# Performance work log

Hardware: AMD Instinct MI355X
Metric: run time of the kernel (lower is better)

## Reference

```python
import jax, jax.numpy as jnp
import numpy as np

NUM_HEADS = 16

def setup_inputs() -> dict:
    key = jax.random.key(0)
    k1, k2, k3 = jax.random.split(key, 3)
    D = 1024
    return {
        "hidden_states": jax.random.normal(k1, (2, 2048, D), dtype=jnp.float32),
        "c_attn_w": jax.random.normal(k2, (D, 3 * D), dtype=jnp.float32) * 0.02,
        "c_attn_b": jnp.zeros((3 * D,), dtype=jnp.float32),
        "c_proj_w": jax.random.normal(k3, (D, D), dtype=jnp.float32) * 0.02,
        "c_proj_b": jnp.zeros((D,), dtype=jnp.float32),
    }

def reference(hidden_states, c_attn_w, c_attn_b, c_proj_w, c_proj_b):
    B, S, D = hidden_states.shape
    H = NUM_HEADS
    hd = D // H
    # Conv1D: x @ W + b, then split into q, k, v
    qkv = hidden_states @ c_attn_w + c_attn_b  # [B, S, 3D]
    q, k, v = jnp.split(qkv, 3, axis=-1)
    q = q.reshape(B, S, H, hd).transpose(0, 2, 1, 3)  # [B, H, S, hd]
    k = k.reshape(B, S, H, hd).transpose(0, 2, 1, 3)
    v = v.reshape(B, S, H, hd).transpose(0, 2, 1, 3)
    # scaled QK^T
    scores = jnp.einsum("bhqd,bhkd->bhqk", q, k) / jnp.asarray(hd ** 0.5, q.dtype)
    # causal mask (tril), masked positions set to dtype min per original code
    causal = jnp.tril(jnp.ones((S, S), dtype=bool))
    mask_value = jnp.finfo(scores.dtype).min
    scores = jnp.where(causal[None, None], scores, mask_value)
    attn = jax.nn.softmax(scores, axis=-1)
    out = jnp.einsum("bhqk,bhkd->bhqd", attn, v)  # [B, H, S, hd]
    out = out.transpose(0, 2, 1, 3).reshape(B, S, D)
    out = out @ c_proj_w + c_proj_b
    return out
```

## Files before the change

### kernel.cpp

```cpp
#include <hip/hip_runtime.h>
#include <hip/hip_bf16.h>
#include <math.h>

#define B_ 2
#define S_ 2048
#define D_ 1024
#define H_ 16
#define HD 64
#define M_ (B_ * S_)
#define N_QKV (3 * D_)

typedef short short8 __attribute__((ext_vector_type(8)));
typedef float floatx4 __attribute__((ext_vector_type(4)));

static __device__ __forceinline__ unsigned short f2bf(float x) {
    __hip_bfloat16 h = __float2bfloat16(x);
    unsigned short u;
    __builtin_memcpy(&u, &h, sizeof(u));
    return u;
}
static __device__ __forceinline__ float bf2f(unsigned short b) {
    union { unsigned u; float f; } v; v.u = ((unsigned)b) << 16;
    return v.f;
}
static __device__ __forceinline__ void split2(float x, unsigned short& h, unsigned short& l) {
    h = f2bf(x);
    l = f2bf(x - bf2f(h));
}

static __device__ __forceinline__ void dma16(const void* g, void* l) {
    __builtin_amdgcn_global_load_lds(
        (const __attribute__((address_space(1))) unsigned int*)g,
        (__attribute__((address_space(3))) unsigned int*)l,
        16, 0, 0);
}

__global__ __launch_bounds__(256) void prep_A(
    const float* __restrict__ X,
    unsigned short* __restrict__ Ahi, unsigned short* __restrict__ Alo)
{
    const size_t i = ((size_t)blockIdx.x * 256 + threadIdx.x) * 8;
    float4 a = *(const float4*)(X + i);
    float4 b = *(const float4*)(X + i + 4);
    float xs[8] = {a.x, a.y, a.z, a.w, b.x, b.y, b.z, b.w};
    short8 h, l;
#pragma unroll
    for (int e = 0; e < 8; e++) {
        unsigned short hh, ll;
        split2(xs[e], hh, ll);
        h[e] = (short)hh; l[e] = (short)ll;
    }
    *(short8*)&Ahi[i] = h;
    *(short8*)&Alo[i] = l;
}

__global__ __launch_bounds__(256) void prep_wT(
    const float* __restrict__ W, int N,
    unsigned short* __restrict__ Thi, unsigned short* __restrict__ Tlo)
{
    __shared__ float Ws[64][68];
    const int t  = threadIdx.x;
    const int n0 = blockIdx.x * 64, k0 = blockIdx.y * 64;
    {
        const int kl = t >> 4, nl = (t & 15) * 4;
        const float* src = W + (size_t)(k0 + kl) * N + n0 + nl;
#pragma unroll
        for (int g = 0; g < 4; g++)
            *(float4*)&Ws[kl + g * 16][nl] = *(const float4*)(src + (size_t)g * 16 * N);
    }
    __syncthreads();
    {
        const int nl = t >> 2, ks = (t & 3) * 16;
        short8 h0, h1, l0, l1;
#pragma unroll
        for (int j = 0; j < 8; j++) {
            unsigned short hh, ll;
            split2(Ws[ks + j][nl], hh, ll);
            h0[j] = (short)hh; l0[j] = (short)ll;
        }
#pragma unroll
        for (int j = 0; j < 8; j++) {
            unsigned short hh, ll;
            split2(Ws[ks + 8 + j][nl], hh, ll);
            h1[j] = (short)hh; l1[j] = (short)ll;
        }
        unsigned short* dh = Thi + (size_t)(n0 + nl) * D_ + k0 + ks;
        unsigned short* dl = Tlo + (size_t)(n0 + nl) * D_ + k0 + ks;
        *(short8*)dh = h0; *(short8*)(dh + 8) = h1;
        *(short8*)dl = l0; *(short8*)(dl + 8) = l1;
    }
}

__global__ __launch_bounds__(256) void gemm_qkv(
    const unsigned short* __restrict__ Ahi, const unsigned short* __restrict__ Alo,
    const unsigned short* __restrict__ BThi, const unsigned short* __restrict__ BTlo,
    const float* __restrict__ bias,
    unsigned short* __restrict__ Qhi, unsigned short* __restrict__ Qlo,
    unsigned short* __restrict__ Khi, unsigned short* __restrict__ Klo,
    unsigned short* __restrict__ vThi, unsigned short* __restrict__ vTlo)
{
    __shared__ unsigned short sAh[128 * 32], sAl[128 * 32];
    __shared__ unsigned short sBh[128 * 32], sBl[128 * 32];

    const int t    = threadIdx.x;
    const int m0   = blockIdx.y * 128, n0 = blockIdx.x * 128;
    const int lane = t & 63, wave = t >> 6;
    const int lm   = lane & 15, quad = lane >> 4;
    const int wm   = (wave >> 1) * 64, wn = (wave & 1) * 64;

    const int lrow = lane >> 2, lcol = (lane & 3) * 8;
    const unsigned short* gAh = Ahi + (size_t)(m0 + wave * 32 + lrow) * D_ + lcol;
    const unsigned short* gAl = Alo + (size_t)(m0 + wave * 32 + lrow) * D_ + lcol;
    const unsigned short* gBh = BThi + (size_t)(n0 + wave * 32 + lrow) * D_ + lcol;
    const unsigned short* gBl = BTlo + (size_t)(n0 + wave * 32 + lrow) * D_ + lcol;
    const int ldst = wave * 1024 + lane * 8;

    floatx4 acc[4][4];
#pragma unroll
    for (int i = 0; i < 4; i++)
#pragma unroll
        for (int j = 0; j < 4; j++)
#pragma unroll
            for (int r = 0; r < 4; r++) acc[i][j][r] = 0.f;

    for (int k0 = 0; k0 < D_; k0 += 32) {
        __syncthreads();
        dma16(gAh + k0, &sAh[ldst]);
        dma16(gAh + (size_t)16 * D_ + k0, &sAh[ldst + 512]);
        dma16(gAl + k0, &sAl[ldst]);
        dma16(gAl + (size_t)16 * D_ + k0, &sAl[ldst + 512]);
        dma16(gBh + k0, &sBh[ldst]);
        dma16(gBh + (size_t)16 * D_ + k0, &sBh[ldst + 512]);
        dma16(gBl + k0, &sBl[ldst]);
        dma16(gBl + (size_t)16 * D_ + k0, &sBl[ldst + 512]);
        __syncthreads();

        short8 bhf[4], blf[4];
#pragma unroll
        for (int nb = 0; nb < 4; nb++) {
            const int r = wn + nb * 16 + lm;
            bhf[nb] = *(const short8*)&sBh[r * 32 + quad * 8];
            blf[nb] = *(const short8*)&sBl[r * 32 + quad * 8];
        }
#pragma unroll
        for (int mb = 0; mb < 4; mb++) {
            const int r = wm + mb * 16 + lm;
            short8 ah = *(const short8*)&sAh[r * 32 + quad * 8];
            short8 al = *(const short8*)&sAl[r * 32 + quad * 8];
#pragma unroll
            for (int nb = 0; nb < 4; nb++) {
                acc[mb][nb] = __builtin_amdgcn_mfma_f32_16x16x32_bf16(ah, bhf[nb], acc[mb][nb], 0, 0, 0);
                acc[mb][nb] = __builtin_amdgcn_mfma_f32_16x16x32_bf16(al, bhf[nb], acc[mb][nb], 0, 0, 0);
                acc[mb][nb] = __builtin_amdgcn_mfma_f32_16x16x32_bf16(ah, blf[nb], acc[mb][nb], 0, 0, 0);
            }
        }
    }

    const int nmode = n0 >> 10;
    if (nmode == 0) {
#pragma unroll
        for (int nb = 0; nb < 4; nb++) {
            const int c = n0 + wn + nb * 16 + lm;
            const float bv = bias[c];
#pragma unroll
            for (int mb = 0; mb < 4; mb++) {
                const int rowb = m0 + wm + mb * 16 + quad * 4;
#pragma unroll
                for (int r = 0; r < 4; r++) {
                    unsigned short hh, ll;
                    split2((acc[mb][nb][r] + bv) * 0.125f, hh, ll);
                    Qhi[(size_t)(rowb + r) * D_ + c] = hh;
                    Qlo[(size_t)(rowb + r) * D_ + c] = ll;
                }
            }
        }
    } else if (nmode == 1) {
#pragma unroll
        for (int nb = 0; nb < 4; nb++) {
            const int c = n0 + wn + nb * 16 + lm;
            const float bv = bias[c];
            const int cq = c - 1024;
#pragma unroll
            for (int mb = 0; mb < 4; mb++) {
                const int rowb = m0 + wm + mb * 16 + quad * 4;
#pragma unroll
                for (int r = 0; r < 4; r++) {
                    unsigned short hh, ll;
                    split2(acc[mb][nb][r] + bv, hh, ll);
                    Khi[(size_t)(rowb + r) * D_ + cq] = hh;
                    Klo[(size_t)(rowb + r) * D_ + cq] = ll;
                }
            }
        }
    } else {
#pragma unroll
        for (int nb = 0; nb < 4; nb++) {
            const int c = n0 + wn + nb * 16 + lm;
            const float bv = bias[c];
            const int cq = c - 2048;
            const int hh_ = cq >> 6, dd = cq & 63;
#pragma unroll
            for (int mb = 0; mb < 4; mb++) {
                const int rowb = m0 + wm + mb * 16 + quad * 4;
                const int bb = rowb >> 11, ss = rowb & 2047;
                unsigned short hv[4], lv[4];
#pragma unroll
                for (int r = 0; r < 4; r++)
                    split2(acc[mb][nb][r] + bv, hv[r], lv[r]);
                const size_t idx = ((size_t)((bb * 16 + hh_) * 64 + dd)) * S_ + ss;
                *(uint2*)&vThi[idx] = make_uint2((unsigned)hv[0] | ((unsigned)hv[1] << 16),
                                                 (unsigned)hv[2] | ((unsigned)hv[3] << 16));
                *(uint2*)&vTlo[idx] = make_uint2((unsigned)lv[0] | ((unsigned)lv[1] << 16),
                                                 (unsigned)lv[2] | ((unsigned)lv[3] << 16));
            }
        }
    }
}

__global__ __launch_bounds__(256) void gemm_out(
    const unsigned short* __restrict__ Ahi, const unsigned short* __restrict__ Alo,
    const unsigned short* __restrict__ BThi, const unsigned short* __restrict__ BTlo,
    const float* __restrict__ bias, float* __restrict__ C)
{
    __shared__ unsigned short sAh[64 * 32], sAl[64 * 32];
    __shared__ unsigned short sBh[64 * 32], sBl[64 * 32];

    const int t   = threadIdx.x;
    const int lid = blockIdx.x;
    const int swz = (lid & 7) * 128 + (lid >> 3);
    const int bx  = swz & 15, by = swz >> 4;
    const int m0  = by * 64, n0 = bx * 64;
    const int lane = t & 63, wave = t >> 6;
    const int lm   = lane & 15, quad = lane >> 4;

    const int lrow = lane >> 2, lcol = (lane & 3) * 8;
    const unsigned short* gAh = Ahi + (size_t)(m0 + wave * 16 + lrow) * D_ + lcol;
    const unsigned short* gAl = Alo + (size_t)(m0 + wave * 16 + lrow) * D_ + lcol;
    const unsigned short* gBh = BThi + (size_t)(n0 + wave * 16 + lrow) * D_ + lcol;
    const unsigned short* gBl = BTlo + (size_t)(n0 + wave * 16 + lrow) * D_ + lcol;
    unsigned short* lAh = sAh + wave * 512 + lane * 8;
    unsigned short* lAl = sAl + wave * 512 + lane * 8;
    unsigned short* lBh = sBh + wave * 512 + lane * 8;
    unsigned short* lBl = sBl + wave * 512 + lane * 8;

    floatx4 acc[4];
#pragma unroll
    for (int j = 0; j < 4; j++)
#pragma unroll
        for (int r = 0; r < 4; r++) acc[j][r] = 0.f;

    for (int k0 = 0; k0 < D_; k0 += 32) {
        __syncthreads();
        dma16(gAh + k0, lAh);
        dma16(gAl + k0, lAl);
        dma16(gBh + k0, lBh);
        dma16(gBl + k0, lBl);
        __syncthreads();

        short8 ah = *(const short8*)&sAh[(wave * 16 + lm) * 32 + quad * 8];
        short8 al = *(const short8*)&sAl[(wave * 16 + lm) * 32 + quad * 8];
#pragma unroll
        for (int nb = 0; nb < 4; nb++) {
            short8 bh = *(const short8*)&sBh[(nb * 16 + lm) * 32 + quad * 8];
            short8 bl = *(const short8*)&sBl[(nb * 16 + lm) * 32 + quad * 8];
            acc[nb] = __builtin_amdgcn_mfma_f32_16x16x32_bf16(ah, bh, acc[nb], 0, 0, 0);
            acc[nb] = __builtin_amdgcn_mfma_f32_16x16x32_bf16(al, bh, acc[nb], 0, 0, 0);
            acc[nb] = __builtin_amdgcn_mfma_f32_16x16x32_bf16(ah, bl, acc[nb], 0, 0, 0);
        }
    }

#pragma unroll
    for (int nb = 0; nb < 4; nb++) {
        const int col = n0 + nb * 16 + lm;
        const float bv = bias[col];
#pragma unroll
        for (int r = 0; r < 4; r++) {
            const int row = m0 + wave * 16 + quad * 4 + r;
            C[(size_t)row * D_ + col] = acc[nb][r] + bv;
        }
    }
}

#define PST 72

__global__ __launch_bounds__(256, 2) void flash_attn_mfma(
    unsigned short* QAhi, unsigned short* QAlo,
    const unsigned short* __restrict__ Khi, const unsigned short* __restrict__ Klo,
    const unsigned short* __restrict__ vThi, const unsigned short* __restrict__ vTlo)
{
    __shared__ unsigned short KhS[64 * PST], KlS[64 * PST];
    __shared__ unsigned short VhS[64 * PST], VlS[64 * PST];
    __shared__ unsigned short PhS[64 * PST], PlS[64 * PST];

    const int t    = threadIdx.x;
    const int pj   = blockIdx.x;
    const int bh   = blockIdx.y;
    const int b    = bh >> 4, h = bh & 15;
    const int lane = t & 63, w = t >> 6;
    const int lm   = lane & 15, quad = lane >> 4;

    const int srow = t >> 2;
    const int sseg = (t & 3) * 16;

    const unsigned short* Kh_b = Khi + (size_t)(b * S_) * D_ + h * HD + sseg;
    const unsigned short* Kl_b = Klo + (size_t)(b * S_) * D_ + h * HD + sseg;
    const unsigned short* Vh_b = vThi + ((size_t)((b * 16 + h) * 64 + srow)) * S_ + sseg;
    const unsigned short* Vl_b = vTlo + ((size_t)((b * 16 + h) * 64 + srow)) * S_ + sseg;

    const int sdst = srow * PST + sseg;

    for (int phse = 0; phse < 2; phse++) {
        const int qt = phse ? (31 - pj) : pj;
        const int q0 = qt * 64;
        const int ntiles = qt + 1;

        short8 qh[2], ql[2];
        {
            const size_t qoff = (size_t)(b * S_ + q0 + 16 * w + lm) * D_ + h * HD + quad * 8;
            qh[0] = *(const short8*)&QAhi[qoff];
            qh[1] = *(const short8*)&QAhi[qoff + 32];
            ql[0] = *(const short8*)&QAlo[qoff];
            ql[1] = *(const short8*)&QAlo[qoff + 32];
        }

        float lsum[4] = {0.f, 0.f, 0.f, 0.f};
        floatx4 o[4];
#pragma unroll
        for (int nb = 0; nb < 4; nb++)
#pragma unroll
            for (int r = 0; r < 4; r++) o[nb][r] = 0.f;

        uint4 pkh0, pkh1, pkl0, pkl1, pvh0, pvh1, pvl0, pvl1;
        pkh0 = *(const uint4*)(Kh_b + (size_t)srow * D_);
        pkh1 = *(const uint4*)(Kh_b + (size_t)srow * D_ + 8);
        pkl0 = *(const uint4*)(Kl_b + (size_t)srow * D_);
        pkl1 = *(const uint4*)(Kl_b + (size_t)srow * D_ + 8);
        pvh0 = *(const uint4*)(Vh_b);
        pvh1 = *(const uint4*)(Vh_b + 8);
        pvl0 = *(const uint4*)(Vl_b);
        pvl1 = *(const uint4*)(Vl_b + 8);

        for (int kt = 0; kt < ntiles; kt++) {
            __syncthreads();
            *(uint4*)&KhS[sdst] = pkh0; *(uint4*)&KhS[sdst + 8] = pkh1;
            *(uint4*)&KlS[sdst] = pkl0; *(uint4*)&KlS[sdst + 8] = pkl1;
            *(uint4*)&VhS[sdst] = pvh0; *(uint4*)&VhS[sdst + 8] = pvh1;
            *(uint4*)&VlS[sdst] = pvl0; *(uint4*)&VlS[sdst + 8] = pvl1;
            __syncthreads();

            if (kt + 1 < ntiles) {
                const int k1 = (kt + 1) * 64;
                pkh0 = *(const uint4*)(Kh_b + (size_t)(k1 + srow) * D_);
                pkh1 = *(const uint4*)(Kh_b + (size_t)(k1 + srow) * D_ + 8);
                pkl0 = *(const uint4*)(Kl_b + (size_t)(k1 + srow) * D_);
                pkl1 = *(const uint4*)(Kl_b + (size_t)(k1 + srow) * D_ + 8);
                pvh0 = *(const uint4*)(Vh_b + k1);
                pvh1 = *(const uint4*)(Vh_b + k1 + 8);
                pvl0 = *(const uint4*)(Vl_b + k1);
                pvl1 = *(const uint4*)(Vl_b + k1 + 8);
            }

            floatx4 sa[4];
#pragma unroll
            for (int nb = 0; nb < 4; nb++)
#pragma unroll
                for (int r = 0; r < 4; r++) sa[nb][r] = 0.f;
            __builtin_amdgcn_s_setprio(1);
#pragma unroll
            for (int s = 0; s < 2; s++) {
#pragma unroll
                for (int nb = 0; nb < 4; nb++) {
                    short8 kh = *(const short8*)&KhS[(nb * 16 + lm) * PST + s * 32 + quad * 8];
                    short8 kl = *(const short8*)&KlS[(nb * 16 + lm) * PST + s * 32 + quad * 8];
                    sa[nb] = __builtin_amdgcn_mfma_f32_16x16x32_bf16(qh[s], kh, sa[nb], 0, 0, 0);
                    sa[nb] = __builtin_amdgcn_mfma_f32_16x16x32_bf16(ql[s], kh, sa[nb], 0, 0, 0);
                    sa[nb] = __builtin_amdgcn_mfma_f32_16x16x32_bf16(qh[s], kl, sa[nb], 0, 0, 0);
                }
            }
            __builtin_amdgcn_s_setprio(0);

            const bool diag = (kt == qt);
            const int kbase = kt * 64;
#pragma unroll
            for (int r = 0; r < 4; r++) {
                const int qabs = q0 + 16 * w + 4 * quad + r;
                const int rloc = 16 * w + 4 * quad + r;
#pragma unroll
                for (int nb = 0; nb < 4; nb++) {
                    float p = __expf(sa[nb][r]);
                    if (diag && (kbase + 16 * nb + lm > qabs)) p = 0.f;
                    lsum[r] += p;
                    unsigned short hh, ll;
                    split2(p, hh, ll);
                    PhS[rloc * PST + 16 * nb + lm] = hh;
                    PlS[rloc * PST + 16 * nb + lm] = ll;
                }
            }

            __builtin_amdgcn_s_setprio(1);
#pragma unroll
            for (int ks = 0; ks < 2; ks++) {
                short8 pf = *(const short8*)&PhS[(16 * w + lm) * PST + ks * 32 + quad * 8];
                short8 pg = *(const short8*)&PlS[(16 * w + lm) * PST + ks * 32 + quad * 8];
#pragma unroll
                for (int nb = 0; nb < 4; nb++) {
                    short8 vhf = *(const short8*)&VhS[(16 * nb + lm) * PST + ks * 32 + quad * 8];
                    short8 vlf = *(const short8*)&VlS[(16 * nb + lm) * PST + ks * 32 + quad * 8];
                    o[nb] = __builtin_amdgcn_mfma_f32_16x16x32_bf16(pf, vhf, o[nb], 0, 0, 0);
                    o[nb] = __builtin_amdgcn_mfma_f32_16x16x32_bf16(pg, vhf, o[nb], 0, 0, 0);
                    o[nb] = __builtin_amdgcn_mfma_f32_16x16x32_bf16(pf, vlf, o[nb], 0, 0, 0);
                }
            }
            __builtin_amdgcn_s_setprio(0);
        }

#pragma unroll
        for (int r = 0; r < 4; r++) {
            float l = lsum[r];
            l += __shfl_xor(l, 1);
            l += __shfl_xor(l, 2);
            l += __shfl_xor(l, 4);
            l += __shfl_xor(l, 8);
            const float inv = 1.f / l;
            const size_t rowoff =
                (size_t)(b * S_ + q0 + 16 * w + 4 * quad + r) * D_ + h * HD + lm;
#pragma unroll
            for (int nb = 0; nb < 4; nb++) {
                unsigned short hh, ll;
                split2(o[nb][r] * inv, hh, ll);
                QAhi[rowoff + 16 * nb] = hh;
                QAlo[rowoff + 16 * nb] = ll;
            }
        }
    }
}

extern "C" void kernel_launch(void* const* d_in, const int* in_sizes, int n_in,
                              void* d_out, int out_size, void* d_ws, size_t ws_size,
                              hipStream_t stream)
{
    const float* hs     = (const float*)d_in[0];
    const float* attn_w = (const float*)d_in[1];
    const float* attn_b = (const float*)d_in[2];
    const float* proj_w = (const float*)d_in[3];
    const float* proj_b = (const float*)d_in[4];
    float* outp = (float*)d_out;

    const size_t QE = (size_t)M_ * D_;
    const size_t WQ = (size_t)D_ * N_QKV;
    unsigned short* Qhi   = (unsigned short*)d_ws;
    unsigned short* Qlo   = Qhi + QE;
    unsigned short* Khi   = Qlo + QE;
    unsigned short* Klo   = Khi + QE;
    unsigned short* vThi  = Klo + QE;
    unsigned short* vTlo  = vThi + QE;
    unsigned short* WqThi = vTlo + QE;
    unsigned short* WqTlo = WqThi + WQ;
    unsigned short* WpThi = WqTlo + WQ;
    unsigned short* WpTlo = WpThi + (size_t)D_ * D_;
    unsigned short* Ahi   = WpTlo + (size_t)D_ * D_;
    unsigned short* Alo   = Ahi + QE;

    dim3 blk(256);
    prep_A<<<dim3(M_ * D_ / 2048), blk, 0, stream>>>(hs, Ahi, Alo);
    prep_wT<<<dim3(N_QKV / 64, D_ / 64), blk, 0, stream>>>(attn_w, N_QKV, WqThi, WqTlo);
    prep_wT<<<dim3(D_ / 64, D_ / 64), blk, 0, stream>>>(proj_w, D_, WpThi, WpTlo);
    gemm_qkv<<<dim3(N_QKV / 128, M_ / 128), blk, 0, stream>>>(
        Ahi, Alo, WqThi, WqTlo, attn_b, Qhi, Qlo, Khi, Klo, vThi, vTlo);
    flash_attn_mfma<<<dim3(16, B_ * H_), dim3(256), 0, stream>>>(
        Qhi, Qlo, Khi, Klo, vThi, vTlo);
    gemm_out<<<dim3(1024), blk, 0, stream>>>(
        Qhi, Qlo, WpThi, WpTlo, proj_b, outp);
}
```

Before: 316.3 us.

## Use 128x128 tiles with split-K atomics in output projection GEMM

The output projection GEMM now uses 128x128 block tiles, with each wave computing a 64x64 sub-tile, and splits K into four 256-wide chunks across grid z. Partial sums are combined with float atomicAdd into an output that a new kernel zeroes first, and the bias is added only by the first split. Larger tiles increase register and LDS reuse per MFMA, and split-K keeps the grid at 1024 blocks despite the larger tiles. The cost is an extra zeroing pass, a 4x atomic read-modify-write traffic on the output, and nondeterministic summation order.

```diff
diff --git a/kernel.cpp b/kernel.cpp
--- a/kernel.cpp
+++ b/kernel.cpp
@@ -33,6 +33,12 @@
         (const __attribute__((address_space(1))) unsigned int*)g,
         (__attribute__((address_space(3))) unsigned int*)l,
         16, 0, 0);
+}
+
+__global__ __launch_bounds__(256) void zero_out(float* __restrict__ C)
+{
+    const size_t i = ((size_t)blockIdx.x * 256 + threadIdx.x) * 4;
+    *(float4*)(C + i) = make_float4(0.f, 0.f, 0.f, 0.f);
 }
 
 __global__ __launch_bounds__(256) void prep_A(
@@ -222,61 +228,75 @@
     const unsigned short* __restrict__ BThi, const unsigned short* __restrict__ BTlo,
     const float* __restrict__ bias, float* __restrict__ C)
 {
-    __shared__ unsigned short sAh[64 * 32], sAl[64 * 32];
-    __shared__ unsigned short sBh[64 * 32], sBl[64 * 32];
-
-    const int t   = threadIdx.x;
-    const int lid = blockIdx.x;
-    const int swz = (lid & 7) * 128 + (lid >> 3);
-    const int bx  = swz & 15, by = swz >> 4;
-    const int m0  = by * 64, n0 = bx * 64;
+    __shared__ unsigned short sAh[128 * 32], sAl[128 * 32];
+    __shared__ unsigned short sBh[128 * 32], sBl[128 * 32];
+
+    const int t     = threadIdx.x;
+    const int m0    = blockIdx.y * 128, n0 = blockIdx.x * 128;
+    const int kbase = blockIdx.z * 256;
     const int lane = t & 63, wave = t >> 6;
     const int lm   = lane & 15, quad = lane >> 4;
+    const int wm   = (wave >> 1) * 64, wn = (wave & 1) * 64;
 
     const int lrow = lane >> 2, lcol = (lane & 3) * 8;
-    const unsigned short* gAh = Ahi + (size_t)(m0 + wave * 16 + lrow) * D_ + lcol;
-    const unsigned short* gAl = Alo + (size_t)(m0 + wave * 16 + lrow) * D_ + lcol;
-    const unsigned short* gBh = BThi + (size_t)(n0 + wave * 16 + lrow) * D_ + lcol;
-    const unsigned short* gBl = BTlo + (size_t)(n0 + wave * 16 + lrow) * D_ + lcol;
-    unsigned short* lAh = sAh + wave * 512 + lane * 8;
-    unsigned short* lAl = sAl + wave * 512 + lane * 8;
-    unsigned short* lBh = sBh + wave * 512 + lane * 8;
-    unsigned short* lBl = sBl + wave * 512 + lane * 8;
-
-    floatx4 acc[4];
-#pragma unroll
-    for (int j = 0; j < 4; j++)
-#pragma unroll
-        for (int r = 0; r < 4; r++) acc[j][r] = 0.f;
-
-    for (int k0 = 0; k0 < D_; k0 += 32) {
+    const unsigned short* gAh = Ahi + (size_t)(m0 + wave * 32 + lrow) * D_ + lcol + kbase;
+    const unsigned short* gAl = Alo + (size_t)(m0 + wave * 32 + lrow) * D_ + lcol + kbase;
+    const unsigned short* gBh = BThi + (size_t)(n0 + wave * 32 + lrow) * D_ + lcol + kbase;
+    const unsigned short* gBl = BTlo + (size_t)(n0 + wave * 32 + lrow) * D_ + lcol + kbase;
+    const int ldst = wave * 1024 + lane * 8;
+
+    floatx4 acc[4][4];
+#pragma unroll
+    for (int i = 0; i < 4; i++)
+#pragma unroll
+        for (int j = 0; j < 4; j++)
+#pragma unroll
+            for (int r = 0; r < 4; r++) acc[i][j][r] = 0.f;
+
+    for (int k0 = 0; k0 < 256; k0 += 32) {
         __syncthreads();
-        dma16(gAh + k0, lAh);
-        dma16(gAl + k0, lAl);
-        dma16(gBh + k0, lBh);
-        dma16(gBl + k0, lBl);
+        dma16(gAh + k0, &sAh[ldst]);
+        dma16(gAh + (size_t)16 * D_ + k0, &sAh[ldst + 512]);
+        dma16(gAl + k0, &sAl[ldst]);
+        dma16(gAl + (size_t)16 * D_ + k0, &sAl[ldst + 512]);
+        dma16(gBh + k0, &sBh[ldst]);
+        dma16(gBh + (size_t)16 * D_ + k0, &sBh[ldst + 512]);
+        dma16(gBl + k0, &sBl[ldst]);
+        dma16(gBl + (size_t)16 * D_ + k0, &sBl[ldst + 512]);
         __syncthreads();
 
-        short8 ah = *(const short8*)&sAh[(wave * 16 + lm) * 32 + quad * 8];
-        short8 al = *(const short8*)&sAl[(wave * 16 + lm) * 32 + quad * 8];
+        short8 bhf[4], blf[4];
 #pragma unroll
         for (int nb = 0; nb < 4; nb++) {
-            short8 bh = *(const short8*)&sBh[(nb * 16 + lm) * 32 + quad * 8];
-            short8 bl = *(const short8*)&sBl[(nb * 16 + lm) * 32 + quad * 8];
-            acc[nb] = __builtin_amdgcn_mfma_f32_16x16x32_bf16(ah, bh, acc[nb], 0, 0, 0);
-            acc[nb] = __builtin_amdgcn_mfma_f32_16x16x32_bf16(al, bh, acc[nb], 0, 0, 0);
-            acc[nb] = __builtin_amdgcn_mfma_f32_16x16x32_bf16(ah, bl, acc[nb], 0, 0, 0);
-        }
-    }
-
+            const int r = wn + nb * 16 + lm;
+            bhf[nb] = *(const short8*)&sBh[r * 32 + quad * 8];
+            blf[nb] = *(const short8*)&sBl[r * 32 + quad * 8];
+        }
+#pragma unroll
+        for (int mb = 0; mb < 4; mb++) {
+            const int r = wm + mb * 16 + lm;
+            short8 ah = *(const short8*)&sAh[r * 32 + quad * 8];
+            short8 al = *(const short8*)&sAl[r * 32 + quad * 8];
+#pragma unroll
+            for (int nb = 0; nb < 4; nb++) {
+                acc[mb][nb] = __builtin_amdgcn_mfma_f32_16x16x32_bf16(ah, bhf[nb], acc[mb][nb], 0, 0, 0);
+                acc[mb][nb] = __builtin_amdgcn_mfma_f32_16x16x32_bf16(al, bhf[nb], acc[mb][nb], 0, 0, 0);
+                acc[mb][nb] = __builtin_amdgcn_mfma_f32_16x16x32_bf16(ah, blf[nb], acc[mb][nb], 0, 0, 0);
+            }
+        }
+    }
+
+    const float bscale = (blockIdx.z == 0) ? 1.f : 0.f;
 #pragma unroll
     for (int nb = 0; nb < 4; nb++) {
-        const int col = n0 + nb * 16 + lm;
-        const float bv = bias[col];
-#pragma unroll
-        for (int r = 0; r < 4; r++) {
-            const int row = m0 + wave * 16 + quad * 4 + r;
-            C[(size_t)row * D_ + col] = acc[nb][r] + bv;
+        const int c = n0 + wn + nb * 16 + lm;
+        const float bv = bias[c] * bscale;
+#pragma unroll
+        for (int mb = 0; mb < 4; mb++) {
+            const int rowb = m0 + wm + mb * 16 + quad * 4;
+#pragma unroll
+            for (int r = 0; r < 4; r++)
+                atomicAdd(&C[(size_t)(rowb + r) * D_ + c], acc[mb][nb][r] + bv);
         }
     }
 }
@@ -462,6 +482,7 @@
     unsigned short* Alo   = Ahi + QE;
 
     dim3 blk(256);
+    zero_out<<<dim3(M_ * D_ / 1024), blk, 0, stream>>>(outp);
     prep_A<<<dim3(M_ * D_ / 2048), blk, 0, stream>>>(hs, Ahi, Alo);
     prep_wT<<<dim3(N_QKV / 64, D_ / 64), blk, 0, stream>>>(attn_w, N_QKV, WqThi, WqTlo);
     prep_wT<<<dim3(D_ / 64, D_ / 64), blk, 0, stream>>>(proj_w, D_, WpThi, WpTlo);
@@ -469,6 +490,6 @@
         Ahi, Alo, WqThi, WqTlo, attn_b, Qhi, Qlo, Khi, Klo, vThi, vTlo);
     flash_attn_mfma<<<dim3(16, B_ * H_), dim3(256), 0, stream>>>(
         Qhi, Qlo, Khi, Klo, vThi, vTlo);
-    gemm_out<<<dim3(1024), blk, 0, stream>>>(
+    gemm_out<<<dim3(D_ / 128, M_ / 128, 4), blk, 0, stream>>>(
         Qhi, Qlo, WpThi, WpTlo, proj_b, outp);
 }
```

New measurement: 358.4 us. 13.3% more time.

## Load K/V tiles via direct global-to-LDS DMA with XOR swizzle

Applied to the files above, without the earlier changes.

Replaces the register-staged K/V prefetch in the flash attention kernel with direct global-to-LDS 16-byte loads (dma16) into unpadded, XOR-swizzled shared tiles. Fragment reads use the matching swizzle, so padding is no longer needed to avoid bank conflicts. Launch bounds are raised to 3 blocks per CU. The aim is to cut register pressure and VGPR round-trips so occupancy can rise. In exchange, the one-tile-ahead software prefetch is lost: loads are now issued and waited on right before compute, which can expose memory latency. The dma16 helper is assumed to be defined elsewhere.

```diff
diff --git a/kernel.cpp b/kernel.cpp
--- a/kernel.cpp
+++ b/kernel.cpp
@@ -281,16 +281,16 @@
     }
 }
 
-#define PST 72
-
-__global__ __launch_bounds__(256, 2) void flash_attn_mfma(
+#define PSP 72
+
+__global__ __launch_bounds__(256, 3) void flash_attn_mfma(
     unsigned short* QAhi, unsigned short* QAlo,
     const unsigned short* __restrict__ Khi, const unsigned short* __restrict__ Klo,
     const unsigned short* __restrict__ vThi, const unsigned short* __restrict__ vTlo)
 {
-    __shared__ unsigned short KhS[64 * PST], KlS[64 * PST];
-    __shared__ unsigned short VhS[64 * PST], VlS[64 * PST];
-    __shared__ unsigned short PhS[64 * PST], PlS[64 * PST];
+    __shared__ unsigned short KhS[64 * 64], KlS[64 * 64];
+    __shared__ unsigned short VhS[64 * 64], VlS[64 * 64];
+    __shared__ unsigned short PhS[64 * PSP], PlS[64 * PSP];
 
     const int t    = threadIdx.x;
     const int pj   = blockIdx.x;
@@ -299,15 +299,14 @@
     const int lane = t & 63, w = t >> 6;
     const int lm   = lane & 15, quad = lane >> 4;
 
-    const int srow = t >> 2;
-    const int sseg = (t & 3) * 16;
-
-    const unsigned short* Kh_b = Khi + (size_t)(b * S_) * D_ + h * HD + sseg;
-    const unsigned short* Kl_b = Klo + (size_t)(b * S_) * D_ + h * HD + sseg;
-    const unsigned short* Vh_b = vThi + ((size_t)((b * 16 + h) * 64 + srow)) * S_ + sseg;
-    const unsigned short* Vl_b = vTlo + ((size_t)((b * 16 + h) * 64 + srow)) * S_ + sseg;
-
-    const int sdst = srow * PST + sseg;
+    const int r0  = t >> 3;
+    const int seg = (t & 7) ^ (r0 & 7);
+    const unsigned short* gKh = Khi + (size_t)(b * S_ + r0) * D_ + h * HD + 8 * seg;
+    const unsigned short* gKl = Klo + (size_t)(b * S_ + r0) * D_ + h * HD + 8 * seg;
+    const unsigned short* gVh = vThi + ((size_t)((b * 16 + h) * 64 + r0)) * S_ + 8 * seg;
+    const unsigned short* gVl = vTlo + ((size_t)((b * 16 + h) * 64 + r0)) * S_ + 8 * seg;
+    const int ld0 = t * 8;
+    const int swzr = (lm & 7) << 3;
 
     for (int phse = 0; phse < 2; phse++) {
         const int qt = phse ? (31 - pj) : pj;
@@ -330,35 +329,21 @@
 #pragma unroll
             for (int r = 0; r < 4; r++) o[nb][r] = 0.f;
 
-        uint4 pkh0, pkh1, pkl0, pkl1, pvh0, pvh1, pvl0, pvl1;
-        pkh0 = *(const uint4*)(Kh_b + (size_t)srow * D_);
-        pkh1 = *(const uint4*)(Kh_b + (size_t)srow * D_ + 8);
-        pkl0 = *(const uint4*)(Kl_b + (size_t)srow * D_);
-        pkl1 = *(const uint4*)(Kl_b + (size_t)srow * D_ + 8);
-        pvh0 = *(const uint4*)(Vh_b);
-        pvh1 = *(const uint4*)(Vh_b + 8);
-        pvl0 = *(const uint4*)(Vl_b);
-        pvl1 = *(const uint4*)(Vl_b + 8);
-
         for (int kt = 0; kt < ntiles; kt++) {
             __syncthreads();
-            *(uint4*)&KhS[sdst] = pkh0; *(uint4*)&KhS[sdst + 8] = pkh1;
-            *(uint4*)&KlS[sdst] = pkl0; *(uint4*)&KlS[sdst + 8] = pkl1;
-            *(uint4*)&VhS[sdst] = pvh0; *(uint4*)&VhS[sdst + 8] = pvh1;
-            *(uint4*)&VlS[sdst] = pvl0; *(uint4*)&VlS[sdst + 8] = pvl1;
+            {
+                const size_t ko = (size_t)(kt * 64) * D_;
+                const int vo = kt * 64;
+                dma16(gKh + ko,                    &KhS[ld0]);
+                dma16(gKh + ko + (size_t)32 * D_,  &KhS[ld0 + 2048]);
+                dma16(gKl + ko,                    &KlS[ld0]);
+                dma16(gKl + ko + (size_t)32 * D_,  &KlS[ld0 + 2048]);
+                dma16(gVh + vo,                    &VhS[ld0]);
+                dma16(gVh + vo + (size_t)32 * S_,  &VhS[ld0 + 2048]);
+                dma16(gVl + vo,                    &VlS[ld0]);
+                dma16(gVl + vo + (size_t)32 * S_,  &VlS[ld0 + 2048]);
+            }
             __syncthreads();
-
-            if (kt + 1 < ntiles) {
-                const int k1 = (kt + 1) * 64;
-                pkh0 = *(const uint4*)(Kh_b + (size_t)(k1 + srow) * D_);
-                pkh1 = *(const uint4*)(Kh_b + (size_t)(k1 + srow) * D_ + 8);
-                pkl0 = *(const uint4*)(Kl_b + (size_t)(k1 + srow) * D_);
-                pkl1 = *(const uint4*)(Kl_b + (size_t)(k1 + srow) * D_ + 8);
-                pvh0 = *(const uint4*)(Vh_b + k1);
-                pvh1 = *(const uint4*)(Vh_b + k1 + 8);
-                pvl0 = *(const uint4*)(Vl_b + k1);
-                pvl1 = *(const uint4*)(Vl_b + k1 + 8);
-            }
 
             floatx4 sa[4];
 #pragma unroll
@@ -370,8 +355,9 @@
             for (int s = 0; s < 2; s++) {
 #pragma unroll
                 for (int nb = 0; nb < 4; nb++) {
-                    short8 kh = *(const short8*)&KhS[(nb * 16 + lm) * PST + s * 32 + quad * 8];
-                    short8 kl = *(const short8*)&KlS[(nb * 16 + lm) * PST + s * 32 + quad * 8];
+                    const int ka = (nb * 16 + lm) * 64 + ((s * 32 + quad * 8) ^ swzr);
+                    short8 kh = *(const short8*)&KhS[ka];
+                    short8 kl = *(const short8*)&KlS[ka];
                     sa[nb] = __builtin_amdgcn_mfma_f32_16x16x32_bf16(qh[s], kh, sa[nb], 0, 0, 0);
                     sa[nb] = __builtin_amdgcn_mfma_f32_16x16x32_bf16(ql[s], kh, sa[nb], 0, 0, 0);
                     sa[nb] = __builtin_amdgcn_mfma_f32_16x16x32_bf16(qh[s], kl, sa[nb], 0, 0, 0);
@@ -392,20 +378,21 @@
                     lsum[r] += p;
                     unsigned short hh, ll;
                     split2(p, hh, ll);
-                    PhS[rloc * PST + 16 * nb + lm] = hh;
-                    PlS[rloc * PST + 16 * nb + lm] = ll;
+                    PhS[rloc * PSP + 16 * nb + lm] = hh;
+                    PlS[rloc * PSP + 16 * nb + lm] = ll;
                 }
             }
 
             __builtin_amdgcn_s_setprio(1);
 #pragma unroll
             for (int ks = 0; ks < 2; ks++) {
-                short8 pf = *(const short8*)&PhS[(16 * w + lm) * PST + ks * 32 + quad * 8];
-                short8 pg = *(const short8*)&PlS[(16 * w + lm) * PST + ks * 32 + quad * 8];
+                short8 pf = *(const short8*)&PhS[(16 * w + lm) * PSP + ks * 32 + quad * 8];
+                short8 pg = *(const short8*)&PlS[(16 * w + lm) * PSP + ks * 32 + quad * 8];
 #pragma unroll
                 for (int nb = 0; nb < 4; nb++) {
-                    short8 vhf = *(const short8*)&VhS[(16 * nb + lm) * PST + ks * 32 + quad * 8];
-                    short8 vlf = *(const short8*)&VlS[(16 * nb + lm) * PST + ks * 32 + quad * 8];
+                    const int va = (nb * 16 + lm) * 64 + ((ks * 32 + quad * 8) ^ swzr);
+                    short8 vhf = *(const short8*)&VhS[va];
+                    short8 vlf = *(const short8*)&VlS[va];
                     o[nb] = __builtin_amdgcn_mfma_f32_16x16x32_bf16(pf, vhf, o[nb], 0, 0, 0);
                     o[nb] = __builtin_amdgcn_mfma_f32_16x16x32_bf16(pg, vhf, o[nb], 0, 0, 0);
                     o[nb] = __builtin_amdgcn_mfma_f32_16x16x32_bf16(pf, vlf, o[nb], 0, 0, 0);
```

After: 307.2 us. 2.9% less time.
